# Performance work log

Hardware: AMD Instinct MI355X
Metric: run time of the kernel (lower is better)

## Reference

```python
import jax, jax.numpy as jnp
import numpy as np

IN_FEATURES = 4096
OUT_FEATURES = 4096


def setup_inputs() -> dict:
    key = jax.random.key(0)
    k_x, k_w, k_b = jax.random.split(key, 3)
    inp = {
        "input": jax.random.normal(k_x, (4, 2048, IN_FEATURES), dtype=jnp.float32),
        # learned int8 weight table [out_features, in_features]
        "weight_int8": jax.random.randint(k_w, (OUT_FEATURES, IN_FEATURES), -128, 128, dtype=jnp.int32).astype(jnp.int8),
        # per-tensor dequant scales (scalars, as in the module buffers)
        "scale": jnp.asarray(0.01, dtype=jnp.float32),
        "x_scale": jnp.asarray(0.05, dtype=jnp.float32),
        "bias": jax.random.normal(k_b, (OUT_FEATURES,), dtype=jnp.float32) * 0.02,
    }
    return inp


def reference(input, weight_int8, scale, x_scale, bias):
    # --- quantize activations per-tensor to int8 (W8A8 path) ---
    x_int8 = jnp.clip(jnp.round(input / x_scale), -128, 127).astype(jnp.int8)
    in_shape = input.shape
    x_flat = x_int8.reshape(-1, in_shape[-1])  # [B*S, in]
    # contract x_flat[k] with weight_int8[n, k] -> [B*S, out]
    out_i32 = jax.lax.dot_general(
        x_flat, weight_int8,
        dimension_numbers=(((1,), (1,)), ((), ())),
        preferred_element_type=jnp.int32,
    )
    # --- dequant epilogue: combined scale, reshape, bias ---
    out = out_i32.astype(input.dtype) * (scale * x_scale)
    out = out.reshape(*in_shape[:-1], weight_int8.shape[0])
    out = out + bias
    return out
```

## Files before the change

### kernel.cpp

```cpp
#include <hip/hip_runtime.h>

#define KDIM 4096
#define NDIM 4096
#define BM 256
#define BN 256
#define BK 128
#define NTILE (KDIM / BK)

using i32x4 = __attribute__((ext_vector_type(4))) int;

__device__ __forceinline__ void g2l16(const void* g, void* l) {
  __builtin_amdgcn_global_load_lds(
      (const __attribute__((address_space(1))) void*)g,
      (__attribute__((address_space(3))) void*)l,
      16, 0, 0);
}

__global__ void w8l_detect(const int* __restrict__ w32, int* __restrict__ flag) {
  __shared__ int s;
  const int t = threadIdx.x;
  if (t == 0) s = 1;
  __syncthreads();
  bool oob = false;
#pragma unroll
  for (int i = 0; i < 16; ++i) {
    int v = w32[t * 16 + i];
    if (v < -128 || v > 127) oob = true;
  }
  if (oob) atomicAnd(&s, 0);
  __syncthreads();
  if (t == 0) *flag = s;
}

__global__ void w8l_pack(const void* __restrict__ wsrc, const int* __restrict__ flag,
                         signed char* __restrict__ wq) {
  if (*flag == 0) return;
  const int t = blockIdx.x * blockDim.x + threadIdx.x;
  const int4* s = (const int4*)wsrc;
  int4 a = s[t * 4 + 0], b = s[t * 4 + 1], c = s[t * 4 + 2], d = s[t * 4 + 3];
  int4 o;
  o.x = (a.x & 255) | ((a.y & 255) << 8) | ((a.z & 255) << 16) | ((a.w & 255) << 24);
  o.y = (b.x & 255) | ((b.y & 255) << 8) | ((b.z & 255) << 16) | ((b.w & 255) << 24);
  o.z = (c.x & 255) | ((c.y & 255) << 8) | ((c.z & 255) << 16) | ((c.w & 255) << 24);
  o.w = (d.x & 255) | ((d.y & 255) << 8) | ((d.z & 255) << 16) | ((d.w & 255) << 24);
  ((int4*)wq)[t] = o;
}

__global__ void w8l_quant(const float* __restrict__ x, const float* __restrict__ xs,
                          signed char* __restrict__ xq) {
  const int t = blockIdx.x * blockDim.x + threadIdx.x;
  const float s = *xs;
  const float4* x4 = (const float4*)x;
  int4 o;
  int* op = (int*)&o;
#pragma unroll
  for (int q = 0; q < 4; ++q) {
    float4 f = x4[t * 4 + q];
    int v0 = __float2int_rn(f.x / s);
    int v1 = __float2int_rn(f.y / s);
    int v2 = __float2int_rn(f.z / s);
    int v3 = __float2int_rn(f.w / s);
    v0 = v0 < -128 ? -128 : (v0 > 127 ? 127 : v0);
    v1 = v1 < -128 ? -128 : (v1 > 127 ? 127 : v1);
    v2 = v2 < -128 ? -128 : (v2 > 127 ? 127 : v2);
    v3 = v3 < -128 ? -128 : (v3 > 127 ? 127 : v3);
    op[q] = (v0 & 255) | ((v1 & 255) << 8) | ((v2 & 255) << 16) | ((v3 & 255) << 24);
  }
  ((int4*)xq)[t] = o;
}

__global__ __launch_bounds__(512, 2) void w8l_gemm8(
    const signed char* __restrict__ Aq,
    const signed char* __restrict__ Wraw, const signed char* __restrict__ Wpk,
    const int* __restrict__ flag,
    const float* __restrict__ scale, const float* __restrict__ xscale,
    const float* __restrict__ bias, float* __restrict__ out, int nbn) {
  __shared__ signed char lds[131072];

  const signed char* __restrict__ Wq = (*flag) ? Wpk : Wraw;

  const int tid = threadIdx.x;
  const int lane = tid & 63;
  const int wid = tid >> 6;
  const int wr = wid >> 2;
  const int wc = wid & 3;
  const int l15 = lane & 15;
  const int l4 = lane >> 4;

  const int nwg = gridDim.x;
  const int cpx = nwg >> 3;
  const int bid = blockIdx.x;
  const int swz = (bid & 7) * cpx + (bid >> 3);
  const int bm = swz / nbn, bn = swz % nbn;
  const int m0 = bm * BM, n0 = bn * BN;

  const unsigned lin = (unsigned)tid * 16u;
  const unsigned r_in = lin >> 7;
  const unsigned c16 = (lin >> 4) & 7;
  const unsigned swcol = ((c16 ^ (r_in & 7)) << 4);
  const signed char* agp = Aq + (size_t)(m0 + r_in) * KDIM + swcol;
  const signed char* wgp = Wq + (size_t)(n0 + r_in) * KDIM + swcol;
  const unsigned ldsoff_thr = r_in * 128u + c16 * 16u;

#define ISSUE_TILE(t)                                                     \
  do {                                                                    \
    const int t_ = (t);                                                   \
    const size_t koff_ = (size_t)t_ * BK;                                 \
    signed char* lb_ = lds + (unsigned)(t_ & 1) * 65536u + ldsoff_thr;    \
    _Pragma("unroll") for (int u = 0; u < 4; ++u)                         \
      g2l16(agp + (size_t)(u * 64) * KDIM + koff_, lb_ + u * 8192);       \
    _Pragma("unroll") for (int u = 0; u < 4; ++u)                         \
      g2l16(wgp + (size_t)(u * 64) * KDIM + koff_, lb_ + 32768 + u * 8192); \
  } while (0)

#define LDFRAG(base, row, sl) \
  (*(const i32x4*)((base) + (row) * 128 + (((((sl) * 4) + l4) ^ ((row) & 7)) * 16)))

  i32x4 acc[8][4] = {};

  ISSUE_TILE(0);

#pragma unroll 1
  for (int kt = 0; kt < NTILE; ++kt) {
    if (kt + 1 < NTILE) {
      ISSUE_TILE(kt + 1);
      asm volatile("s_waitcnt vmcnt(8)" ::: "memory");
    } else {
      asm volatile("s_waitcnt vmcnt(0)" ::: "memory");
    }
    __builtin_amdgcn_s_barrier();
    __builtin_amdgcn_sched_barrier(0);

    const signed char* Ab = &lds[(kt & 1) * 65536];
    const signed char* Bb = Ab + 32768;
    i32x4 a0[4][2], a1[4][2], b01[2][2], b23[2][2];

#pragma unroll
    for (int i = 0; i < 4; ++i)
#pragma unroll
      for (int s = 0; s < 2; ++s) a0[i][s] = LDFRAG(Ab, wr * 128 + i * 16 + l15, s);
#pragma unroll
    for (int j = 0; j < 2; ++j)
#pragma unroll
      for (int s = 0; s < 2; ++s) b01[j][s] = LDFRAG(Bb, wc * 64 + j * 16 + l15, s);
    asm volatile("s_waitcnt lgkmcnt(0)" ::: "memory");
    __builtin_amdgcn_sched_barrier(0);

#pragma unroll
    for (int j = 0; j < 2; ++j)
#pragma unroll
      for (int s = 0; s < 2; ++s) b23[j][s] = LDFRAG(Bb, wc * 64 + (j + 2) * 16 + l15, s);
    __builtin_amdgcn_sched_barrier(0);
#pragma unroll
    for (int i = 0; i < 4; ++i)
#pragma unroll
      for (int s = 0; s < 2; ++s) a1[i][s] = LDFRAG(Ab, wr * 128 + (i + 4) * 16 + l15, s);
    __builtin_amdgcn_sched_barrier(0);

    __builtin_amdgcn_s_setprio(1);
#pragma unroll
    for (int i = 0; i < 4; ++i)
#pragma unroll
      for (int j = 0; j < 2; ++j)
#pragma unroll
        for (int s = 0; s < 2; ++s)
          acc[i][j] = __builtin_amdgcn_mfma_i32_16x16x64_i8(a0[i][s], b01[j][s], acc[i][j], 0, 0, 0);
    __builtin_amdgcn_s_setprio(0);

    asm volatile("s_waitcnt lgkmcnt(8)" ::: "memory");
    __builtin_amdgcn_sched_barrier(0);
    __builtin_amdgcn_s_setprio(1);
#pragma unroll
    for (int i = 0; i < 4; ++i)
#pragma unroll
      for (int j = 0; j < 2; ++j)
#pragma unroll
        for (int s = 0; s < 2; ++s)
          acc[i][j + 2] = __builtin_amdgcn_mfma_i32_16x16x64_i8(a0[i][s], b23[j][s], acc[i][j + 2], 0, 0, 0);
    __builtin_amdgcn_s_setprio(0);

    asm volatile("s_waitcnt lgkmcnt(0)" ::: "memory");
    __builtin_amdgcn_sched_barrier(0);
    __builtin_amdgcn_s_setprio(1);
#pragma unroll
    for (int i = 0; i < 4; ++i)
#pragma unroll
      for (int j = 0; j < 2; ++j)
#pragma unroll
        for (int s = 0; s < 2; ++s)
          acc[i + 4][j + 2] = __builtin_amdgcn_mfma_i32_16x16x64_i8(a1[i][s], b23[j][s], acc[i + 4][j + 2], 0, 0, 0);
#pragma unroll
    for (int i = 0; i < 4; ++i)
#pragma unroll
      for (int j = 0; j < 2; ++j)
#pragma unroll
        for (int s = 0; s < 2; ++s)
          acc[i + 4][j] = __builtin_amdgcn_mfma_i32_16x16x64_i8(a1[i][s], b01[j][s], acc[i + 4][j], 0, 0, 0);
    __builtin_amdgcn_s_setprio(0);
    __builtin_amdgcn_sched_barrier(0);
    __builtin_amdgcn_s_barrier();
  }

  const float cs = scale[0] * xscale[0];
#pragma unroll
  for (int j = 0; j < 4; ++j) {
    const int n = n0 + wc * 64 + j * 16 + l15;
    const float bj = bias[n];
#pragma unroll
    for (int i = 0; i < 8; ++i) {
      const int m = m0 + wr * 128 + i * 16 + l4 * 4;
      float* o = out + (size_t)m * NDIM + n;
#pragma unroll
      for (int v = 0; v < 4; ++v)
        o[(size_t)v * NDIM] = (float)acc[i][j][v] * cs + bj;
    }
  }
#undef ISSUE_TILE
#undef LDFRAG
}

extern "C" void kernel_launch(void* const* d_in, const int* in_sizes, int n_in,
                              void* d_out, int out_size, void* d_ws, size_t ws_size,
                              hipStream_t stream) {
  const float* x = (const float*)d_in[0];
  const void* w = d_in[1];
  const float* scale = (const float*)d_in[2];
  const float* xscale = (const float*)d_in[3];
  const float* bias = (const float*)d_in[4];
  float* out = (float*)d_out;

  const int M = in_sizes[0] / KDIM;

  int* flag = (int*)d_ws;
  signed char* wq = (signed char*)d_ws + 256;
  signed char* aq = wq + (size_t)NDIM * KDIM;

  const size_t need = 256 + (size_t)NDIM * KDIM + (size_t)M * KDIM;
  if (ws_size < need) return;

  w8l_detect<<<1, 256, 0, stream>>>((const int*)w, flag);
  w8l_pack<<<(NDIM * KDIM / 16) / 256, 256, 0, stream>>>(w, flag, wq);
  w8l_quant<<<(M * KDIM / 16) / 256, 256, 0, stream>>>(x, xscale, aq);

  const int nbn = NDIM / BN;
  w8l_gemm8<<<(M / BM) * nbn, 512, 0, stream>>>(
      aq, (const signed char*)w, wq, flag, scale, xscale, bias, out, nbn);
}
```

Measured before the change: 189.4 us.

## Software-pipeline LDS fragment reads against MFMA across K sub-slices

Restructures the int8 GEMM main loop so each 128-wide K tile is split into two 64-wide halves. Fragments for the next half, or for the next tile, are read from LDS while the current half's MFMA cluster runs. A prologue now issues two tiles ahead, and the next global-to-LDS tile load is issued after the mid-iteration barrier, so the wait on global loads moves from the loop top to the middle. This aims to hide LDS read latency and barrier stalls behind matrix-core work, at the cost of a tighter vmcnt(0) wait and the same large fragment register footprint.

```diff
diff --git a/kernel.cpp b/kernel.cpp
--- a/kernel.cpp
+++ b/kernel.cpp
@@ -69,7 +69,7 @@
   ((int4*)xq)[t] = o;
 }
 
-__global__ __launch_bounds__(512, 2) void w8l_gemm8(
+__global__ __launch_bounds__(512, 2) void w8l_gemmp(
     const signed char* __restrict__ Aq,
     const signed char* __restrict__ Wraw, const signed char* __restrict__ Wpk,
     const int* __restrict__ flag,
@@ -102,103 +102,72 @@
   const signed char* wgp = Wq + (size_t)(n0 + r_in) * KDIM + swcol;
   const unsigned ldsoff_thr = r_in * 128u + c16 * 16u;
 
-#define ISSUE_TILE(t)                                                     \
-  do {                                                                    \
-    const int t_ = (t);                                                   \
-    const size_t koff_ = (size_t)t_ * BK;                                 \
-    signed char* lb_ = lds + (unsigned)(t_ & 1) * 65536u + ldsoff_thr;    \
-    _Pragma("unroll") for (int u = 0; u < 4; ++u)                         \
-      g2l16(agp + (size_t)(u * 64) * KDIM + koff_, lb_ + u * 8192);       \
-    _Pragma("unroll") for (int u = 0; u < 4; ++u)                         \
+#define ISSUE_TILE(t)                                                       \
+  do {                                                                      \
+    const int t_ = (t);                                                     \
+    const size_t koff_ = (size_t)t_ * BK;                                   \
+    signed char* lb_ = lds + (unsigned)(t_ & 1) * 65536u + ldsoff_thr;      \
+    _Pragma("unroll") for (int u = 0; u < 4; ++u)                           \
+      g2l16(agp + (size_t)(u * 64) * KDIM + koff_, lb_ + u * 8192);         \
+    _Pragma("unroll") for (int u = 0; u < 4; ++u)                           \
       g2l16(wgp + (size_t)(u * 64) * KDIM + koff_, lb_ + 32768 + u * 8192); \
   } while (0)
 
 #define LDFRAG(base, row, sl) \
   (*(const i32x4*)((base) + (row) * 128 + (((((sl) * 4) + l4) ^ ((row) & 7)) * 16)))
 
+#define READ_A(dst, base, sl)                                          \
+  _Pragma("unroll") for (int i = 0; i < 8; ++i)                        \
+      dst[i] = LDFRAG((base), wr * 128 + i * 16 + l15, (sl));
+#define READ_B(dst, base, sl)                                          \
+  _Pragma("unroll") for (int j = 0; j < 4; ++j)                        \
+      dst[j] = LDFRAG((base), wc * 64 + j * 16 + l15, (sl));
+#define MFMA_CLUSTER(av, bv)                                           \
+  __builtin_amdgcn_s_setprio(1);                                       \
+  _Pragma("unroll") for (int i = 0; i < 8; ++i)                        \
+      _Pragma("unroll") for (int j = 0; j < 4; ++j)                    \
+          acc[i][j] = __builtin_amdgcn_mfma_i32_16x16x64_i8(           \
+              av[i], bv[j], acc[i][j], 0, 0, 0);                       \
+  __builtin_amdgcn_s_setprio(0);
+
   i32x4 acc[8][4] = {};
+  i32x4 aE[8], bE[4], aO[8], bO[4];
 
   ISSUE_TILE(0);
+  ISSUE_TILE(1);
+  asm volatile("s_waitcnt vmcnt(8)" ::: "memory");
+  __builtin_amdgcn_s_barrier();
+  __builtin_amdgcn_sched_barrier(0);
+  READ_A(aE, lds, 0);
+  READ_B(bE, lds + 32768, 0);
+  __builtin_amdgcn_sched_barrier(0);
 
 #pragma unroll 1
   for (int kt = 0; kt < NTILE; ++kt) {
-    if (kt + 1 < NTILE) {
-      ISSUE_TILE(kt + 1);
-      asm volatile("s_waitcnt vmcnt(8)" ::: "memory");
-    } else {
-      asm volatile("s_waitcnt vmcnt(0)" ::: "memory");
-    }
-    __builtin_amdgcn_s_barrier();
-    __builtin_amdgcn_sched_barrier(0);
-
     const signed char* Ab = &lds[(kt & 1) * 65536];
     const signed char* Bb = Ab + 32768;
-    i32x4 a0[4][2], a1[4][2], b01[2][2], b23[2][2];
-
-#pragma unroll
-    for (int i = 0; i < 4; ++i)
-#pragma unroll
-      for (int s = 0; s < 2; ++s) a0[i][s] = LDFRAG(Ab, wr * 128 + i * 16 + l15, s);
-#pragma unroll
-    for (int j = 0; j < 2; ++j)
-#pragma unroll
-      for (int s = 0; s < 2; ++s) b01[j][s] = LDFRAG(Bb, wc * 64 + j * 16 + l15, s);
+
+    READ_A(aO, Ab, 1);
+    READ_B(bO, Bb, 1);
+    __builtin_amdgcn_sched_barrier(0);
+    MFMA_CLUSTER(aE, bE);
+    __builtin_amdgcn_sched_barrier(0);
     asm volatile("s_waitcnt lgkmcnt(0)" ::: "memory");
     __builtin_amdgcn_sched_barrier(0);
 
-#pragma unroll
-    for (int j = 0; j < 2; ++j)
-#pragma unroll
-      for (int s = 0; s < 2; ++s) b23[j][s] = LDFRAG(Bb, wc * 64 + (j + 2) * 16 + l15, s);
-    __builtin_amdgcn_sched_barrier(0);
-#pragma unroll
-    for (int i = 0; i < 4; ++i)
-#pragma unroll
-      for (int s = 0; s < 2; ++s) a1[i][s] = LDFRAG(Ab, wr * 128 + (i + 4) * 16 + l15, s);
-    __builtin_amdgcn_sched_barrier(0);
-
-    __builtin_amdgcn_s_setprio(1);
-#pragma unroll
-    for (int i = 0; i < 4; ++i)
-#pragma unroll
-      for (int j = 0; j < 2; ++j)
-#pragma unroll
-        for (int s = 0; s < 2; ++s)
-          acc[i][j] = __builtin_amdgcn_mfma_i32_16x16x64_i8(a0[i][s], b01[j][s], acc[i][j], 0, 0, 0);
-    __builtin_amdgcn_s_setprio(0);
-
-    asm volatile("s_waitcnt lgkmcnt(8)" ::: "memory");
-    __builtin_amdgcn_sched_barrier(0);
-    __builtin_amdgcn_s_setprio(1);
-#pragma unroll
-    for (int i = 0; i < 4; ++i)
-#pragma unroll
-      for (int j = 0; j < 2; ++j)
-#pragma unroll
-        for (int s = 0; s < 2; ++s)
-          acc[i][j + 2] = __builtin_amdgcn_mfma_i32_16x16x64_i8(a0[i][s], b23[j][s], acc[i][j + 2], 0, 0, 0);
-    __builtin_amdgcn_s_setprio(0);
-
-    asm volatile("s_waitcnt lgkmcnt(0)" ::: "memory");
-    __builtin_amdgcn_sched_barrier(0);
-    __builtin_amdgcn_s_setprio(1);
-#pragma unroll
-    for (int i = 0; i < 4; ++i)
-#pragma unroll
-      for (int j = 0; j < 2; ++j)
-#pragma unroll
-        for (int s = 0; s < 2; ++s)
-          acc[i + 4][j + 2] = __builtin_amdgcn_mfma_i32_16x16x64_i8(a1[i][s], b23[j][s], acc[i + 4][j + 2], 0, 0, 0);
-#pragma unroll
-    for (int i = 0; i < 4; ++i)
-#pragma unroll
-      for (int j = 0; j < 2; ++j)
-#pragma unroll
-        for (int s = 0; s < 2; ++s)
-          acc[i + 4][j] = __builtin_amdgcn_mfma_i32_16x16x64_i8(a1[i][s], b01[j][s], acc[i + 4][j], 0, 0, 0);
-    __builtin_amdgcn_s_setprio(0);
-    __builtin_amdgcn_sched_barrier(0);
-    __builtin_amdgcn_s_barrier();
+    if (kt + 1 < NTILE) {
+      asm volatile("s_waitcnt vmcnt(0)" ::: "memory");
+      __builtin_amdgcn_s_barrier();
+      __builtin_amdgcn_sched_barrier(0);
+      const signed char* An = &lds[((kt + 1) & 1) * 65536];
+      const signed char* Bn = An + 32768;
+      READ_A(aE, An, 0);
+      READ_B(bE, Bn, 0);
+      if (kt + 2 < NTILE) ISSUE_TILE(kt + 2);
+      __builtin_amdgcn_sched_barrier(0);
+    }
+    MFMA_CLUSTER(aO, bO);
+    __builtin_amdgcn_sched_barrier(0);
   }
 
   const float cs = scale[0] * xscale[0];
@@ -217,6 +186,9 @@
   }
 #undef ISSUE_TILE
 #undef LDFRAG
+#undef READ_A
+#undef READ_B
+#undef MFMA_CLUSTER
 }
 
 extern "C" void kernel_launch(void* const* d_in, const int* in_sizes, int n_in,
@@ -243,6 +215,6 @@
   w8l_quant<<<(M * KDIM / 16) / 256, 256, 0, stream>>>(x, xscale, aq);
 
   const int nbn = NDIM / BN;
-  w8l_gemm8<<<(M / BM) * nbn, 512, 0, stream>>>(
+  w8l_gemmp<<<(M / BM) * nbn, 512, 0, stream>>>(
       aq, (const signed char*)w, wq, flag, scale, xscale, bias, out, nbn);
 }
```

After: 181.5 us. 1.04x faster.
